# Performance work log

Measured on AMD Instinct MI355X. Metric: run time of the kernel, lower is better.

The kernel has to match this reference:

```python
import jax, jax.numpy as jnp
import numpy as np

TEMPERATURE = 8.0  # sqrt(d_k=64)


def setup_inputs() -> dict:
    key = jax.random.key(0)
    kq, kk, kv = jax.random.split(key, 3)
    B, H, L, D = 4, 16, 2048, 64
    q = jax.random.normal(kq, (B, H, L, D), dtype=jnp.float32)
    k = jax.random.normal(kk, (B, H, L, D), dtype=jnp.float32)
    v = jax.random.normal(kv, (B, H, L, D), dtype=jnp.float32)
    return {"q": q, "k": k, "v": v}


def reference(q, k, v):
    # attn = softmax((q/T) @ k^T)  over last axis; dropout is identity in eval
    scores = jnp.einsum("bhqd,bhkd->bhqk", q / TEMPERATURE, k)
    attn = jax.nn.softmax(scores, axis=-1)
    out = jnp.einsum("bhqk,bhkd->bhqd", attn, v)
    return (out, attn)
```

## Files before the change

kernel.cpp:

```cpp
#include <hip/hip_runtime.h>
#include <hip/hip_bf16.h>

typedef __attribute__((ext_vector_type(4))) float  f32x4;
typedef __attribute__((ext_vector_type(8))) short  bf16x8;
typedef __attribute__((ext_vector_type(4))) short  bf16x4;

#define MFMA16(a, b, c) __builtin_amdgcn_mfma_f32_16x16x32_bf16((a), (b), (c), 0, 0, 0)

__device__ __forceinline__ short f2bf(float f) {
  return __builtin_bit_cast(short, __float2bfloat16(f));
}
__device__ __forceinline__ float bf2f(short b) {
  return __builtin_bit_cast(float, ((unsigned)(unsigned short)b) << 16);
}

__device__ __forceinline__ void sync_lds() {
  asm volatile("s_waitcnt lgkmcnt(0)" ::: "memory");
  __builtin_amdgcn_s_barrier();
  asm volatile("" ::: "memory");
}

constexpr int L = 2048, D = 64, KT = 64, NT = L / KT;
constexpr int NHEAD = 64;
constexpr int QB = 128, NQT = L / QB;
constexpr float QSCALE = 0.18033688011112042f;
constexpr size_t BF_ELEMS = (size_t)NHEAD * L * D;
constexpr size_t WS_NEED = 3 * BF_ELEMS * sizeof(short) + (size_t)NHEAD * L * sizeof(float);

__global__ __launch_bounds__(256)
void sdpa_prep(const float* __restrict__ Q, const float* __restrict__ K,
               const float* __restrict__ V,
               short* __restrict__ Qb, short* __restrict__ Kb,
               short* __restrict__ Vtb)
{
  __shared__ short Tl[64 * 72];
  const int t = threadIdx.x;
  const int head = blockIdx.x >> 5, kt = blockIdx.x & 31;
  const long base = (long)head * L * D + (long)kt * 64 * D;

  {
    const float* qp = Q + base + t * 16;
    short*       qo = Qb + base + t * 16;
    bf16x8 y0, y1;
    #pragma unroll
    for (int j = 0; j < 8; ++j) {
      y0[j] = f2bf(qp[j]     * QSCALE);
      y1[j] = f2bf(qp[8 + j] * QSCALE);
    }
    *(bf16x8*)qo = y0; *(bf16x8*)(qo + 8) = y1;
  }
  {
    const float* kp = K + base + t * 16;
    short*       ko = Kb + base + t * 16;
    bf16x8 y0, y1;
    #pragma unroll
    for (int j = 0; j < 8; ++j) { y0[j] = f2bf(kp[j]); y1[j] = f2bf(kp[8 + j]); }
    *(bf16x8*)ko = y0; *(bf16x8*)(ko + 8) = y1;
  }
  {
    const int kr0 = (t >> 4) * 4, d0 = (t & 15) * 4;
    const float* vp = V + base;
    f32x4 r[4];
    #pragma unroll
    for (int i = 0; i < 4; ++i) r[i] = *(const f32x4*)(vp + (kr0 + i) * D + d0);
    #pragma unroll
    for (int j = 0; j < 4; ++j) {
      bf16x4 y;
      #pragma unroll
      for (int i = 0; i < 4; ++i) y[i] = f2bf(r[i][j]);
      *(bf16x4*)(&Tl[(d0 + j) * 72 + kr0]) = y;
    }
  }
  __syncthreads();
  {
    const int d = t >> 2, k0 = (t & 3) * 16;
    bf16x8 a = *(const bf16x8*)(&Tl[d * 72 + k0]);
    bf16x8 b = *(const bf16x8*)(&Tl[d * 72 + k0 + 8]);
    short* vo = Vtb + (long)head * D * L + (long)d * L + kt * 64 + k0;
    *(bf16x8*)vo = a; *(bf16x8*)(vo + 8) = b;
  }
}

__global__ __launch_bounds__(256, 4)
void sdpa_rowsum(const short* __restrict__ Qb, const short* __restrict__ Kb,
                 float* __restrict__ rinv_out)
{
  __shared__ short Klds[2][KT * D];

  const int t = threadIdx.x, lane = t & 63, w = t >> 6;
  const int qr = lane & 15, g = lane >> 4;

  const int bid = blockIdx.x;
  const int wid = ((bid & 7) << 7) | (bid >> 3);
  const int head = wid >> 4, qt = wid & 15;
  const long hoff = (long)head * L * D;
  const int qrow0 = qt * QB + w * 32;

  bf16x8 qfrag[2][2];
  #pragma unroll
  for (int h = 0; h < 2; ++h) {
    const short* qbp = Qb + hoff + (long)(qrow0 + 16 * h + qr) * D + g * 8;
    qfrag[h][0] = *(const bf16x8*)qbp;
    qfrag[h][1] = *(const bf16x8*)(qbp + 32);
  }

  const short* Kbase = Kb + hoff;
  bf16x8 kreg[2];
  const int krow = t >> 2, kd0 = (t & 3) * 16;

  auto loadK = [&](int kt) {
    const short* kp = Kbase + (long)(kt * KT + krow) * D + kd0;
    kreg[0] = *(const bf16x8*)kp;
    kreg[1] = *(const bf16x8*)(kp + 8);
  };
  auto writeK = [&](int buf) {
    const int sw = (krow & 7) << 3;
    *(bf16x8*)(&Klds[buf][krow * 64 + (kd0 ^ sw)])       = kreg[0];
    *(bf16x8*)(&Klds[buf][krow * 64 + ((kd0 + 8) ^ sw)]) = kreg[1];
  };

  loadK(0); writeK(0);
  sync_lds();
  float rsum0 = 0.f, rsum1 = 0.f;
  for (int kt = 0; kt < NT; ++kt) {
    const int cur = kt & 1;
    if (kt + 1 < NT) loadK(kt + 1);
    #pragma unroll
    for (int f = 0; f < 4; ++f) {
      f32x4 s0 = (f32x4){0.f,0.f,0.f,0.f};
      f32x4 s1 = (f32x4){0.f,0.f,0.f,0.f};
      int kr = f * 16 + qr;
      #pragma unroll
      for (int c = 0; c < 2; ++c) {
        int d0c = g * 8 + 32 * c;
        bf16x8 a = *(const bf16x8*)(&Klds[cur][kr * 64 + (d0c ^ ((kr & 7) << 3))]);
        s0 = MFMA16(a, qfrag[0][c], s0);
        s1 = MFMA16(a, qfrag[1][c], s1);
      }
      #pragma unroll
      for (int r = 0; r < 4; ++r) {
        rsum0 += __builtin_amdgcn_exp2f(s0[r]);
        rsum1 += __builtin_amdgcn_exp2f(s1[r]);
      }
    }
    if (kt + 1 < NT) writeK(cur ^ 1);
    sync_lds();
  }
  rsum0 += __shfl_xor(rsum0, 16); rsum0 += __shfl_xor(rsum0, 32);
  rsum1 += __shfl_xor(rsum1, 16); rsum1 += __shfl_xor(rsum1, 32);
  if (lane < 16) {
    float* ro = rinv_out + (long)head * L + qrow0;
    ro[qr]      = 1.f / rsum0;
    ro[16 + qr] = 1.f / rsum1;
  }
}

__global__ __launch_bounds__(256, 4)
void sdpa_main(const short* __restrict__ Qb, const short* __restrict__ Kb,
               const short* __restrict__ Vtb, const float* __restrict__ rinv_ws,
               float* __restrict__ out, float* __restrict__ attn)
{
  __shared__ short Klds[2][KT * D];
  __shared__ short Vlds[2][D * KT];
  __shared__ short Plds[4][16 * KT];

  const int t = threadIdx.x, lane = t & 63, w = t >> 6;
  const int qr = lane & 15, g = lane >> 4;

  const int bid = blockIdx.x;
  const int wid = ((bid & 7) << 7) | (bid >> 3);
  const int head = wid >> 4, qt = wid & 15;
  const long hoff = (long)head * L * D;
  const int qrow0 = qt * QB + w * 32;

  const float rinv0 = rinv_ws[(long)head * L + qrow0 + qr];
  const float rinv1 = rinv_ws[(long)head * L + qrow0 + 16 + qr];

  bf16x8 qfrag[2][2];
  #pragma unroll
  for (int h = 0; h < 2; ++h) {
    const short* qbp = Qb + hoff + (long)(qrow0 + 16 * h + qr) * D + g * 8;
    qfrag[h][0] = *(const bf16x8*)qbp;
    qfrag[h][1] = *(const bf16x8*)(qbp + 32);
  }

  const short* Kbase = Kb + hoff;
  const short* Vbase = Vtb + (long)head * D * L;

  bf16x8 kreg[2], vreg[2];
  const int krow = t >> 2, kd0 = (t & 3) * 16;

  auto loadK = [&](int kt) {
    const short* kp = Kbase + (long)(kt * KT + krow) * D + kd0;
    kreg[0] = *(const bf16x8*)kp;
    kreg[1] = *(const bf16x8*)(kp + 8);
  };
  auto writeK = [&](int buf) {
    const int sw = (krow & 7) << 3;
    *(bf16x8*)(&Klds[buf][krow * 64 + (kd0 ^ sw)])       = kreg[0];
    *(bf16x8*)(&Klds[buf][krow * 64 + ((kd0 + 8) ^ sw)]) = kreg[1];
  };
  auto loadV = [&](int kt) {
    const short* vp = Vbase + (long)krow * L + kt * KT + kd0;
    vreg[0] = *(const bf16x8*)vp;
    vreg[1] = *(const bf16x8*)(vp + 8);
  };
  auto writeV = [&](int buf) {
    const int sw = (krow & 7) << 3;
    *(bf16x8*)(&Vlds[buf][krow * 64 + (kd0 ^ sw)])       = vreg[0];
    *(bf16x8*)(&Vlds[buf][krow * 64 + ((kd0 + 8) ^ sw)]) = vreg[1];
  };

  auto computeS2 = [&](int buf, f32x4 s0[4], f32x4 s1[4]) {
    #pragma unroll
    for (int f = 0; f < 4; ++f) {
      s0[f] = (f32x4){0.f, 0.f, 0.f, 0.f};
      s1[f] = (f32x4){0.f, 0.f, 0.f, 0.f};
      int kr = f * 16 + qr;
      #pragma unroll
      for (int c = 0; c < 2; ++c) {
        int d0c = g * 8 + 32 * c;
        bf16x8 a = *(const bf16x8*)(&Klds[buf][kr * 64 + (d0c ^ ((kr & 7) << 3))]);
        s0[f] = MFMA16(a, qfrag[0][c], s0[f]);
        s1[f] = MFMA16(a, qfrag[1][c], s1[f]);
      }
    }
  };

  f32x4 o0[4] = {{0.f,0.f,0.f,0.f},{0.f,0.f,0.f,0.f},{0.f,0.f,0.f,0.f},{0.f,0.f,0.f,0.f}};
  f32x4 o1[4] = {{0.f,0.f,0.f,0.f},{0.f,0.f,0.f,0.f},{0.f,0.f,0.f,0.f},{0.f,0.f,0.f,0.f}};
  float* ap0 = attn + (long)head * L * L + (long)(qrow0 + qr) * L;
  float* ap1 = ap0 + 16 * L;

  auto doHalf = [&](f32x4 s[4], float rinv, float* ap, f32x4 o[4], int cur, int kt) {
    #pragma unroll
    for (int f = 0; f < 4; ++f) {
      f32x4 pf;
      #pragma unroll
      for (int r = 0; r < 4; ++r)
        pf[r] = __builtin_amdgcn_exp2f(s[f][r]) * rinv;
      *(f32x4*)(ap + kt * KT + f * 16 + g * 4) = pf;
      bf16x4 p;
      #pragma unroll
      for (int r = 0; r < 4; ++r) p[r] = f2bf(pf[r]);
      int k0 = f * 16 + g * 4;
      *(bf16x4*)(&Plds[w][qr * 64 + (k0 ^ ((qr & 7) << 3))]) = p;
    }
    __builtin_amdgcn_wave_barrier();
    #pragma unroll
    for (int kc = 0; kc < 2; ++kc) {
      int k0 = kc * 32 + g * 8;
      bf16x8 pa = *(const bf16x8*)(&Plds[w][qr * 64 + (k0 ^ ((qr & 7) << 3))]);
      #pragma unroll
      for (int fr = 0; fr < 4; ++fr) {
        int d = fr * 16 + qr;
        bf16x8 vb = *(const bf16x8*)(&Vlds[cur][d * 64 + (k0 ^ ((d & 7) << 3))]);
        o[fr] = MFMA16(pa, vb, o[fr]);
      }
    }
    __builtin_amdgcn_wave_barrier();
  };

  loadK(0); loadV(0);
  writeK(0); writeV(0);
  sync_lds();

  for (int kt = 0; kt < NT; ++kt) {
    const int cur = kt & 1;
    if (kt + 1 < NT) { loadK(kt + 1); loadV(kt + 1); }

    f32x4 s0[4], s1[4];
    computeS2(cur, s0, s1);

    doHalf(s0, rinv0, ap0, o0, cur, kt);
    doHalf(s1, rinv1, ap1, o1, cur, kt);

    if (kt + 1 < NT) { writeK(cur ^ 1); writeV(cur ^ 1); }
    sync_lds();
  }

  float* op = out + hoff + (long)qrow0 * D;
  #pragma unroll
  for (int fr = 0; fr < 4; ++fr)
    #pragma unroll
    for (int r = 0; r < 4; ++r) {
      op[(long)(g * 4 + r) * D + fr * 16 + qr]      = o0[fr][r];
      op[(long)(16 + g * 4 + r) * D + fr * 16 + qr] = o1[fr][r];
    }
}

__global__ __launch_bounds__(256, 4)
void sdpa_fused(const float* __restrict__ Q, const float* __restrict__ K,
                const float* __restrict__ V, float* __restrict__ out,
                float* __restrict__ attn)
{
  __shared__ short Klds[2][KT * D];
  __shared__ short Vlds[2][D * KT];
  __shared__ short Plds[4][16 * KT];

  const int t = threadIdx.x, lane = t & 63, w = t >> 6;
  const int qr = lane & 15, g = lane >> 4;
  const int head = blockIdx.x >> 5, qt = blockIdx.x & 31;
  const long hoff = (long)head * L * D;
  const int qrow0 = qt * 64 + w * 16;

  bf16x8 qfrag[2];
  {
    const float* qp = Q + hoff + (long)(qrow0 + qr) * D + g * 8;
    #pragma unroll
    for (int c = 0; c < 2; ++c)
      #pragma unroll
      for (int j = 0; j < 8; ++j)
        qfrag[c][j] = f2bf(qp[32 * c + j] * QSCALE);
  }

  const float* Kbase = K + hoff;
  const float* Vbase = V + hoff;
  f32x4 kreg[4], vreg[4];

  auto loadK = [&](int kt) {
    const float* kp = Kbase + (long)kt * KT * D;
    #pragma unroll
    for (int c = 0; c < 4; ++c)
      kreg[c] = *(const f32x4*)(kp + (t + 256 * c) * 4);
  };
  auto writeK = [&](int buf) {
    #pragma unroll
    for (int c = 0; c < 4; ++c) {
      int f = t + 256 * c;
      int kr = f >> 4, col = (f & 15) * 4;
      bf16x4 y;
      #pragma unroll
      for (int i = 0; i < 4; ++i) y[i] = f2bf(kreg[c][i]);
      *(bf16x4*)(&Klds[buf][kr * 64 + (col ^ ((kr & 7) << 3))]) = y;
    }
  };
  auto loadV = [&](int kt) {
    const float* vp = Vbase + (long)kt * KT * D;
    int kr0 = (t >> 4) * 4, d0 = (t & 15) * 4;
    #pragma unroll
    for (int i = 0; i < 4; ++i)
      vreg[i] = *(const f32x4*)(vp + (kr0 + i) * D + d0);
  };
  auto writeV = [&](int buf) {
    int kr0 = (t >> 4) * 4, d0 = (t & 15) * 4;
    #pragma unroll
    for (int j = 0; j < 4; ++j) {
      bf16x4 y;
      #pragma unroll
      for (int i = 0; i < 4; ++i) y[i] = f2bf(vreg[i][j]);
      int d = d0 + j;
      *(bf16x4*)(&Vlds[buf][d * 64 + (kr0 ^ ((d & 7) << 3))]) = y;
    }
  };
  auto computeS = [&](int buf, f32x4 s[4]) {
    #pragma unroll
    for (int f = 0; f < 4; ++f) {
      s[f] = (f32x4){0.f, 0.f, 0.f, 0.f};
      int kr = f * 16 + qr;
      #pragma unroll
      for (int c = 0; c < 2; ++c) {
        int d0c = g * 8 + 32 * c;
        bf16x8 a = *(const bf16x8*)(&Klds[buf][kr * 64 + (d0c ^ ((kr & 7) << 3))]);
        s[f] = MFMA16(a, qfrag[c], s[f]);
      }
    }
  };

  loadK(0); writeK(0);
  sync_lds();
  float rsum = 0.f;
  for (int kt = 0; kt < NT; ++kt) {
    const int cur = kt & 1;
    if (kt + 1 < NT) loadK(kt + 1);
    f32x4 s[4];
    computeS(cur, s);
    #pragma unroll
    for (int f = 0; f < 4; ++f)
      #pragma unroll
      for (int r = 0; r < 4; ++r)
        rsum += __builtin_amdgcn_exp2f(s[f][r]);
    if (kt + 1 < NT) writeK(cur ^ 1);
    sync_lds();
  }
  rsum += __shfl_xor(rsum, 16);
  rsum += __shfl_xor(rsum, 32);
  const float rinv = 1.f / rsum;

  f32x4 o[4] = {{0.f,0.f,0.f,0.f},{0.f,0.f,0.f,0.f},{0.f,0.f,0.f,0.f},{0.f,0.f,0.f,0.f}};
  float* ap_base = attn + (long)head * L * L + (long)qrow0 * L;

  loadK(0); loadV(0);
  writeK(0); writeV(0);
  sync_lds();

  for (int kt = 0; kt < NT; ++kt) {
    const int cur = kt & 1;
    if (kt + 1 < NT) { loadK(kt + 1); loadV(kt + 1); }

    f32x4 s[4];
    computeS(cur, s);

    #pragma unroll
    for (int f = 0; f < 4; ++f) {
      bf16x4 p;
      #pragma unroll
      for (int r = 0; r < 4; ++r)
        p[r] = f2bf(__builtin_amdgcn_exp2f(s[f][r]) * rinv);
      int k0 = f * 16 + g * 4;
      *(bf16x4*)(&Plds[w][qr * 64 + (k0 ^ ((qr & 7) << 3))]) = p;
    }
    __builtin_amdgcn_wave_barrier();

    float* ap = ap_base + (long)kt * KT;
    #pragma unroll
    for (int i = 0; i < 4; ++i) {
      int r = 4 * i + g, col = 4 * qr;
      bf16x4 pb = *(const bf16x4*)(&Plds[w][r * 64 + (col ^ ((r & 7) << 3))]);
      f32x4 pf;
      #pragma unroll
      for (int j = 0; j < 4; ++j) pf[j] = bf2f(pb[j]);
      *(f32x4*)(ap + (long)r * L + col) = pf;
    }

    #pragma unroll
    for (int kc = 0; kc < 2; ++kc) {
      int k0 = kc * 32 + g * 8;
      bf16x8 pa = *(const bf16x8*)(&Plds[w][qr * 64 + (k0 ^ ((qr & 7) << 3))]);
      #pragma unroll
      for (int fr = 0; fr < 4; ++fr) {
        int d = fr * 16 + qr;
        bf16x8 vb = *(const bf16x8*)(&Vlds[cur][d * 64 + (k0 ^ ((d & 7) << 3))]);
        o[fr] = MFMA16(pa, vb, o[fr]);
      }
    }

    if (kt + 1 < NT) { writeK(cur ^ 1); writeV(cur ^ 1); }
    sync_lds();
  }

  float* op = out + hoff + (long)qrow0 * D;
  #pragma unroll
  for (int fr = 0; fr < 4; ++fr)
    #pragma unroll
    for (int r = 0; r < 4; ++r) {
      int qq = g * 4 + r;
      op[(long)qq * D + fr * 16 + qr] = o[fr][r];
    }
}

extern "C" void kernel_launch(void* const* d_in, const int* in_sizes, int n_in,
                              void* d_out, int out_size, void* d_ws, size_t ws_size,
                              hipStream_t stream) {
  const float* q = (const float*)d_in[0];
  const float* k = (const float*)d_in[1];
  const float* v = (const float*)d_in[2];
  float* out  = (float*)d_out;
  float* attn = (float*)d_out + (size_t)NHEAD * L * D;

  dim3 block(256);

  if (ws_size >= WS_NEED) {
    short* Qb   = (short*)d_ws;
    short* Kb   = Qb + BF_ELEMS;
    short* Vtb  = Kb + BF_ELEMS;
    float* rinv = (float*)(Vtb + BF_ELEMS);
    hipLaunchKernelGGL(sdpa_prep,   dim3(NHEAD * NT),  block, 0, stream, q, k, v, Qb, Kb, Vtb);
    hipLaunchKernelGGL(sdpa_rowsum, dim3(NHEAD * NQT), block, 0, stream, Qb, Kb, rinv);
    hipLaunchKernelGGL(sdpa_main,   dim3(NHEAD * NQT), block, 0, stream, Qb, Kb, Vtb, rinv, out, attn);
  } else {
    hipLaunchKernelGGL(sdpa_fused, dim3(NHEAD * NT), block, 0, stream, q, k, v, out, attn);
  }
}
```

Baseline: 354.2 us.

## Fuse Q/K bf16 conversion into rowsum kernel, keep prep for V only

Moves the fp32-to-bf16 conversion of Q and K out of the prep kernel and into the rowsum pass. The rowsum pass now reads fp32 Q and K directly and converts them in registers. Each block also writes its slice of bf16 Q and K to the workspace for the main kernel to use. This removes a separate read-write pass over Q and K and part of the prep launch. In exchange, rowsum reads fp32 K, which is twice the bytes of bf16, for every K tile across all 16 query tiles, raising its global traffic.

```diff
diff --git a/kernel.cpp b/kernel.cpp
--- a/kernel.cpp
+++ b/kernel.cpp
@@ -28,62 +28,37 @@
 constexpr size_t WS_NEED = 3 * BF_ELEMS * sizeof(short) + (size_t)NHEAD * L * sizeof(float);
 
 __global__ __launch_bounds__(256)
-void sdpa_prep(const float* __restrict__ Q, const float* __restrict__ K,
-               const float* __restrict__ V,
-               short* __restrict__ Qb, short* __restrict__ Kb,
-               short* __restrict__ Vtb)
+void sdpa_prepV(const float* __restrict__ V, short* __restrict__ Vtb)
 {
   __shared__ short Tl[64 * 72];
   const int t = threadIdx.x;
   const int head = blockIdx.x >> 5, kt = blockIdx.x & 31;
   const long base = (long)head * L * D + (long)kt * 64 * D;
 
-  {
-    const float* qp = Q + base + t * 16;
-    short*       qo = Qb + base + t * 16;
-    bf16x8 y0, y1;
-    #pragma unroll
-    for (int j = 0; j < 8; ++j) {
-      y0[j] = f2bf(qp[j]     * QSCALE);
-      y1[j] = f2bf(qp[8 + j] * QSCALE);
-    }
-    *(bf16x8*)qo = y0; *(bf16x8*)(qo + 8) = y1;
-  }
-  {
-    const float* kp = K + base + t * 16;
-    short*       ko = Kb + base + t * 16;
-    bf16x8 y0, y1;
-    #pragma unroll
-    for (int j = 0; j < 8; ++j) { y0[j] = f2bf(kp[j]); y1[j] = f2bf(kp[8 + j]); }
-    *(bf16x8*)ko = y0; *(bf16x8*)(ko + 8) = y1;
-  }
-  {
-    const int kr0 = (t >> 4) * 4, d0 = (t & 15) * 4;
-    const float* vp = V + base;
-    f32x4 r[4];
-    #pragma unroll
-    for (int i = 0; i < 4; ++i) r[i] = *(const f32x4*)(vp + (kr0 + i) * D + d0);
-    #pragma unroll
-    for (int j = 0; j < 4; ++j) {
-      bf16x4 y;
-      #pragma unroll
-      for (int i = 0; i < 4; ++i) y[i] = f2bf(r[i][j]);
-      *(bf16x4*)(&Tl[(d0 + j) * 72 + kr0]) = y;
-    }
+  const int kr0 = (t >> 4) * 4, d0 = (t & 15) * 4;
+  const float* vp = V + base;
+  f32x4 r[4];
+  #pragma unroll
+  for (int i = 0; i < 4; ++i) r[i] = *(const f32x4*)(vp + (kr0 + i) * D + d0);
+  #pragma unroll
+  for (int j = 0; j < 4; ++j) {
+    bf16x4 y;
+    #pragma unroll
+    for (int i = 0; i < 4; ++i) y[i] = f2bf(r[i][j]);
+    *(bf16x4*)(&Tl[(d0 + j) * 72 + kr0]) = y;
   }
   __syncthreads();
-  {
-    const int d = t >> 2, k0 = (t & 3) * 16;
-    bf16x8 a = *(const bf16x8*)(&Tl[d * 72 + k0]);
-    bf16x8 b = *(const bf16x8*)(&Tl[d * 72 + k0 + 8]);
-    short* vo = Vtb + (long)head * D * L + (long)d * L + kt * 64 + k0;
-    *(bf16x8*)vo = a; *(bf16x8*)(vo + 8) = b;
-  }
+  const int d = t >> 2, k0 = (t & 3) * 16;
+  bf16x8 a = *(const bf16x8*)(&Tl[d * 72 + k0]);
+  bf16x8 b = *(const bf16x8*)(&Tl[d * 72 + k0 + 8]);
+  short* vo = Vtb + (long)head * D * L + (long)d * L + kt * 64 + k0;
+  *(bf16x8*)vo = a; *(bf16x8*)(vo + 8) = b;
 }
 
 __global__ __launch_bounds__(256, 4)
-void sdpa_rowsum(const short* __restrict__ Qb, const short* __restrict__ Kb,
-                 float* __restrict__ rinv_out)
+void sdpa_rowsum2(const float* __restrict__ Qf, const float* __restrict__ Kf,
+                  short* __restrict__ Qb, short* __restrict__ Kb,
+                  float* __restrict__ rinv_out)
 {
   __shared__ short Klds[2][KT * D];
 
@@ -96,30 +71,70 @@
   const long hoff = (long)head * L * D;
   const int qrow0 = qt * QB + w * 32;
 
+  {
+    const float* qp = Qf + hoff + (long)qt * QB * D + t * 32;
+    short*       qo = Qb + hoff + (long)qt * QB * D + t * 32;
+    #pragma unroll
+    for (int c = 0; c < 4; ++c) {
+      f32x4 a = *(const f32x4*)(qp + c * 8);
+      f32x4 b = *(const f32x4*)(qp + c * 8 + 4);
+      bf16x8 y;
+      #pragma unroll
+      for (int j = 0; j < 4; ++j) {
+        y[j]     = f2bf(a[j] * QSCALE);
+        y[4 + j] = f2bf(b[j] * QSCALE);
+      }
+      *(bf16x8*)(qo + c * 8) = y;
+    }
+  }
+
   bf16x8 qfrag[2][2];
   #pragma unroll
-  for (int h = 0; h < 2; ++h) {
-    const short* qbp = Qb + hoff + (long)(qrow0 + 16 * h + qr) * D + g * 8;
-    qfrag[h][0] = *(const bf16x8*)qbp;
-    qfrag[h][1] = *(const bf16x8*)(qbp + 32);
-  }
-
-  const short* Kbase = Kb + hoff;
-  bf16x8 kreg[2];
+  for (int h = 0; h < 2; ++h)
+    #pragma unroll
+    for (int c = 0; c < 2; ++c) {
+      const float* qp = Qf + hoff + (long)(qrow0 + 16 * h + qr) * D + g * 8 + 32 * c;
+      f32x4 a = *(const f32x4*)qp;
+      f32x4 b = *(const f32x4*)(qp + 4);
+      #pragma unroll
+      for (int j = 0; j < 4; ++j) {
+        qfrag[h][c][j]     = f2bf(a[j] * QSCALE);
+        qfrag[h][c][4 + j] = f2bf(b[j] * QSCALE);
+      }
+    }
+
+  const float* KfH = Kf + hoff;
+  short*       KbH = Kb + hoff;
   const int krow = t >> 2, kd0 = (t & 3) * 16;
+  f32x4 kf[4];
+  bf16x8 kb0, kb1;
 
   auto loadK = [&](int kt) {
-    const short* kp = Kbase + (long)(kt * KT + krow) * D + kd0;
-    kreg[0] = *(const bf16x8*)kp;
-    kreg[1] = *(const bf16x8*)(kp + 8);
-  };
-  auto writeK = [&](int buf) {
+    const float* kp = KfH + (long)(kt * KT + krow) * D + kd0;
+    #pragma unroll
+    for (int i = 0; i < 4; ++i) kf[i] = *(const f32x4*)(kp + 4 * i);
+  };
+  auto cvtK = [&]() {
+    #pragma unroll
+    for (int j = 0; j < 8; ++j) {
+      kb0[j] = f2bf(kf[j >> 2][j & 3]);
+      kb1[j] = f2bf(kf[2 + (j >> 2)][j & 3]);
+    }
+  };
+  auto writeKlds = [&](int buf) {
     const int sw = (krow & 7) << 3;
-    *(bf16x8*)(&Klds[buf][krow * 64 + (kd0 ^ sw)])       = kreg[0];
-    *(bf16x8*)(&Klds[buf][krow * 64 + ((kd0 + 8) ^ sw)]) = kreg[1];
-  };
-
-  loadK(0); writeK(0);
+    *(bf16x8*)(&Klds[buf][krow * 64 + (kd0 ^ sw)])       = kb0;
+    *(bf16x8*)(&Klds[buf][krow * 64 + ((kd0 + 8) ^ sw)]) = kb1;
+  };
+  auto maybeWriteKb = [&](int kt) {
+    if ((kt >> 1) == qt) {
+      short* ko = KbH + (long)(kt * KT + krow) * D + kd0;
+      *(bf16x8*)ko = kb0;
+      *(bf16x8*)(ko + 8) = kb1;
+    }
+  };
+
+  loadK(0); cvtK(); writeKlds(0); maybeWriteKb(0);
   sync_lds();
   float rsum0 = 0.f, rsum1 = 0.f;
   for (int kt = 0; kt < NT; ++kt) {
@@ -143,7 +158,7 @@
         rsum1 += __builtin_amdgcn_exp2f(s1[r]);
       }
     }
-    if (kt + 1 < NT) writeK(cur ^ 1);
+    if (kt + 1 < NT) { cvtK(); writeKlds(cur ^ 1); maybeWriteKb(kt + 1); }
     sync_lds();
   }
   rsum0 += __shfl_xor(rsum0, 16); rsum0 += __shfl_xor(rsum0, 32);
@@ -465,9 +480,9 @@
     short* Kb   = Qb + BF_ELEMS;
     short* Vtb  = Kb + BF_ELEMS;
     float* rinv = (float*)(Vtb + BF_ELEMS);
-    hipLaunchKernelGGL(sdpa_prep,   dim3(NHEAD * NT),  block, 0, stream, q, k, v, Qb, Kb, Vtb);
-    hipLaunchKernelGGL(sdpa_rowsum, dim3(NHEAD * NQT), block, 0, stream, Qb, Kb, rinv);
-    hipLaunchKernelGGL(sdpa_main,   dim3(NHEAD * NQT), block, 0, stream, Qb, Kb, Vtb, rinv, out, attn);
+    hipLaunchKernelGGL(sdpa_prepV,   dim3(NHEAD * NT),  block, 0, stream, v, Vtb);
+    hipLaunchKernelGGL(sdpa_rowsum2, dim3(NHEAD * NQT), block, 0, stream, q, k, Qb, Kb, rinv);
+    hipLaunchKernelGGL(sdpa_main,    dim3(NHEAD * NQT), block, 0, stream, Qb, Kb, Vtb, rinv, out, attn);
   } else {
     hipLaunchKernelGGL(sdpa_fused, dim3(NHEAD * NT), block, 0, stream, q, k, v, out, attn);
   }
```

Result: no change. 359.7 us (+1.5%).
